# Optimization experiments

Hardware: AMD Instinct MI355X
Metric: run time of the kernel (lower is better)

Reference implementation:

```python
import jax, jax.numpy as jnp
import numpy as np

POOL_SIZE = 7
CROP = POOL_SIZE * 2  # if_max_pool=True -> crop to 14x14 then 2x2 max-pool


def setup_inputs() -> dict:
    key = jax.random.key(0)
    k1, k2, k3 = jax.random.split(key, 3)
    H, W, C = 50, 75, 512          # VGG conv5 features of an 800x1200 image (stride 16)
    N = 1000                       # post-NMS RPN proposals
    feature_map = jax.random.normal(k1, (1, H, W, C), dtype=jnp.float32)
    img_size = jnp.array([800, 1200], dtype=jnp.int32)
    # rois in pixel coords (x1, y1, x2, y2), guaranteed x1<=x2, y1<=y2, in-bounds
    xs = jax.random.uniform(k2, (N, 2), minval=0.0, maxval=1199.0)
    ys = jax.random.uniform(k3, (N, 2), minval=0.0, maxval=799.0)
    rois = jnp.stack([xs.min(1), ys.min(1), xs.max(1), ys.max(1)], axis=1).astype(jnp.float32)
    return {"feature_map": feature_map, "rois": rois, "img_size": img_size}


def _crop_and_resize(feature_map, boxes, crop_h, crop_w):
    """tf.image.crop_and_resize (bilinear) with all box_indices == 0.
    feature_map: (1,H,W,C); boxes: (N,4) normalized [y1,x1,y2,x2].
    Returns (N, crop_h, crop_w, C).
    """
    H, W = feature_map.shape[1], feature_map.shape[2]
    img = feature_map[0]  # (H,W,C)
    y1, x1, y2, x2 = boxes[:, 0], boxes[:, 1], boxes[:, 2], boxes[:, 3]
    fh, fw = jnp.float32(H - 1), jnp.float32(W - 1)
    iy = jnp.arange(crop_h, dtype=jnp.float32)
    ix = jnp.arange(crop_w, dtype=jnp.float32)
    # in-image sample coords (crop size > 1 branch of TF semantics)
    ys = y1[:, None] * fh + iy[None, :] * ((y2 - y1) * fh / (crop_h - 1))[:, None]  # (N,ch)
    xs = x1[:, None] * fw + ix[None, :] * ((x2 - x1) * fw / (crop_w - 1))[:, None]  # (N,cw)
    valid = ((ys >= 0) & (ys <= fh))[:, :, None] & ((xs >= 0) & (xs <= fw))[:, None, :]  # (N,ch,cw)
    y0 = jnp.floor(ys); x0 = jnp.floor(xs)
    wy = (ys - y0)[:, :, None, None]   # (N,ch,1,1)
    wx = (xs - x0)[:, None, :, None]   # (N,1,cw,1)
    y0i = jnp.clip(y0.astype(jnp.int32), 0, H - 1)
    x0i = jnp.clip(x0.astype(jnp.int32), 0, W - 1)
    y1i = jnp.clip(y0i + 1, 0, H - 1)
    x1i = jnp.clip(x0i + 1, 0, W - 1)
    # per-ROI bilinear gather: (N,ch,cw,C)
    tl = img[y0i[:, :, None], x0i[:, None, :]]
    tr = img[y0i[:, :, None], x1i[:, None, :]]
    bl = img[y1i[:, :, None], x0i[:, None, :]]
    br = img[y1i[:, :, None], x1i[:, None, :]]
    top = tl + wx * (tr - tl)
    bot = bl + wx * (br - bl)
    val = top + wy * (bot - top)
    return jnp.where(valid[..., None], val, 0.0)


def reference(feature_map, rois, img_size):
    img_h = img_size[0].astype(jnp.float32) - 1.0
    img_w = img_size[1].astype(jnp.float32) - 1.0
    boxes = jnp.stack([rois[:, 1] / img_h, rois[:, 0] / img_w,
                       rois[:, 3] / img_h, rois[:, 2] / img_w], axis=1)
    boxes = jax.lax.stop_gradient(boxes)
    crops = _crop_and_resize(feature_map, boxes, CROP, CROP)  # (N,14,14,C)
    N, _, _, C = crops.shape
    # MaxPool2D((2,2), padding='same'); 14 is even so 'same' == 'valid' reshape trick
    return crops.reshape(N, POOL_SIZE, 2, POOL_SIZE, 2, C).max(axis=(2, 4))
```

## Files before the change

### kernel.cpp

```cpp
#include <hip/hip_runtime.h>

#define FH 50
#define FW 75
#define FC 512
#define NPOOL 7
#define NXCD 8

typedef float f32x4 __attribute__((ext_vector_type(4)));

__device__ __forceinline__ float uniform_f(float x) {
    return __int_as_float(__builtin_amdgcn_readfirstlane(__float_as_int(x)));
}

__global__ __launch_bounds__(128) void roi_pool_kernel(
    const float* __restrict__ fmap,
    const float* __restrict__ rois,
    const int*   __restrict__ img_size,
    float* __restrict__ out,
    int N)
{
    const int nwg = gridDim.x;
    const int q = nwg / NXCD, r = nwg % NXCD;
    const int xcd = blockIdx.x % NXCD, local = blockIdx.x / NXCD;
    const int w = (xcd < r ? xcd * (q + 1) : r * (q + 1) + (xcd - r) * q) + local;

    const int n  = w / (NPOOL * NPOOL);
    const int p  = w % (NPOOL * NPOOL);
    const int py = p / NPOOL;
    const int px = p % NPOOL;
    if (n >= N) return;

    const float img_h = (float)(img_size[0] - 1);
    const float img_w = (float)(img_size[1] - 1);

    const float rx1 = rois[n * 4 + 0];
    const float ry1 = rois[n * 4 + 1];
    const float rx2 = rois[n * 4 + 2];
    const float ry2 = rois[n * 4 + 3];

    const float fh = (float)(FH - 1);
    const float fw = (float)(FW - 1);
    const float stepy = (ry2 - ry1) / img_h * fh * (1.0f / 13.0f);
    const float stepx = (rx2 - rx1) / img_w * fw * (1.0f / 13.0f);
    const float basey = ry1 / img_h * fh;
    const float basex = rx1 / img_w * fw;

    int   off00[4], off01[4], off10[4], off11[4];
    float w00_[4], w01_[4], w10_[4], w11_[4];
    #pragma unroll
    for (int kk = 0; kk < 4; ++kk) {
        const int iy = py * 2 + (kk >> 1);
        const int ix = px * 2 + (kk & 1);
        const float ys = basey + (float)iy * stepy;
        const float xs = basex + (float)ix * stepx;
        const float mv = ((ys >= 0.0f) & (ys <= fh) & (xs >= 0.0f) & (xs <= fw))
                         ? 1.0f : 0.0f;

        const float y0f = floorf(ys);
        const float x0f = floorf(xs);
        const float wy = ys - y0f;
        const float wx = xs - x0f;
        int y0i = (int)y0f; y0i = min(max(y0i, 0), FH - 1);
        int x0i = (int)x0f; x0i = min(max(x0i, 0), FW - 1);
        const int y1i = min(y0i + 1, FH - 1);
        const int x1i = min(x0i + 1, FW - 1);

        w00_[kk] = uniform_f((1.0f - wy) * (1.0f - wx) * mv);
        w01_[kk] = uniform_f((1.0f - wy) * wx * mv);
        w10_[kk] = uniform_f(wy * (1.0f - wx) * mv);
        w11_[kk] = uniform_f(wy * wx * mv);

        off00[kk] = __builtin_amdgcn_readfirstlane((y0i * FW + x0i) * FC);
        off01[kk] = __builtin_amdgcn_readfirstlane((y0i * FW + x1i) * FC);
        off10[kk] = __builtin_amdgcn_readfirstlane((y1i * FW + x0i) * FC);
        off11[kk] = __builtin_amdgcn_readfirstlane((y1i * FW + x1i) * FC);
    }

    const int c4 = threadIdx.x * 4;
    const float* fm = fmap + c4;

    f32x4 tl0, tr0, bl0, br0, tl1, tr1, bl1, br1;
    f32x4 tl2, tr2, bl2, br2, tl3, tr3, bl3, br3;
    tl0 = *(const f32x4*)(fm + off00[0]);
    tr0 = *(const f32x4*)(fm + off01[0]);
    bl0 = *(const f32x4*)(fm + off10[0]);
    br0 = *(const f32x4*)(fm + off11[0]);
    tl1 = *(const f32x4*)(fm + off00[1]);
    tr1 = *(const f32x4*)(fm + off01[1]);
    bl1 = *(const f32x4*)(fm + off10[1]);
    br1 = *(const f32x4*)(fm + off11[1]);
    tl2 = *(const f32x4*)(fm + off00[2]);
    tr2 = *(const f32x4*)(fm + off01[2]);
    bl2 = *(const f32x4*)(fm + off10[2]);
    br2 = *(const f32x4*)(fm + off11[2]);
    tl3 = *(const f32x4*)(fm + off00[3]);
    tr3 = *(const f32x4*)(fm + off01[3]);
    bl3 = *(const f32x4*)(fm + off10[3]);
    br3 = *(const f32x4*)(fm + off11[3]);

    asm volatile("" : "+v"(tl0), "+v"(tr0), "+v"(bl0), "+v"(br0),
                      "+v"(tl1), "+v"(tr1), "+v"(bl1), "+v"(br1),
                      "+v"(tl2), "+v"(tr2), "+v"(bl2), "+v"(br2),
                      "+v"(tl3), "+v"(tr3), "+v"(bl3), "+v"(br3));

    const f32x4 v0 = w00_[0] * tl0 + w01_[0] * tr0 + w10_[0] * bl0 + w11_[0] * br0;
    const f32x4 v1 = w00_[1] * tl1 + w01_[1] * tr1 + w10_[1] * bl1 + w11_[1] * br1;
    const f32x4 v2 = w00_[2] * tl2 + w01_[2] * tr2 + w10_[2] * bl2 + w11_[2] * br2;
    const f32x4 v3 = w00_[3] * tl3 + w01_[3] * tr3 + w10_[3] * bl3 + w11_[3] * br3;

    f32x4 m;
    m.x = fmaxf(fmaxf(fmaxf(v0.x, v1.x), v2.x), v3.x);
    m.y = fmaxf(fmaxf(fmaxf(v0.y, v1.y), v2.y), v3.y);
    m.z = fmaxf(fmaxf(fmaxf(v0.z, v1.z), v2.z), v3.z);
    m.w = fmaxf(fmaxf(fmaxf(v0.w, v1.w), v2.w), v3.w);

    f32x4* dst = (f32x4*)(out + (((long)n * NPOOL + py) * NPOOL + px) * FC + c4);
    __builtin_nontemporal_store(m, dst);
}

extern "C" void kernel_launch(void* const* d_in, const int* in_sizes, int n_in,
                              void* d_out, int out_size, void* d_ws, size_t ws_size,
                              hipStream_t stream) {
    const float* fmap     = (const float*)d_in[0];
    const float* rois     = (const float*)d_in[1];
    const int*   img_size = (const int*)d_in[2];
    float* out = (float*)d_out;

    const int N = in_sizes[1] / 4;
    const int blocks = N * NPOOL * NPOOL;
    roi_pool_kernel<<<blocks, 128, 0, stream>>>(fmap, rois, img_size, out, N);
}
```

Measured before the change: 159.4 us.

## Precompute separable per-ROI row/column sample tables in a setup kernel

```diff
diff --git a/kernel.cpp b/kernel.cpp
--- a/kernel.cpp
+++ b/kernel.cpp
@@ -5,17 +5,70 @@
 #define FC 512
 #define NPOOL 7
 #define NXCD 8
+#define NSAMP 14
 
 typedef float f32x4 __attribute__((ext_vector_type(4)));
+typedef int   i32x4 __attribute__((ext_vector_type(4)));
 
-__device__ __forceinline__ float uniform_f(float x) {
-    return __int_as_float(__builtin_amdgcn_readfirstlane(__float_as_int(x)));
+__global__ __launch_bounds__(256) void roi_setup_kernel(
+    const float* __restrict__ rois,
+    const int*   __restrict__ img_size,
+    i32x4* __restrict__ tab,
+    int N)
+{
+    const int idx = blockIdx.x * 256 + threadIdx.x;
+    const int total = N * NSAMP;
+    if (idx >= 2 * total) return;
+
+    const bool is_col = idx >= total;
+    const int  e = is_col ? idx - total : idx;
+    const int  n = e / NSAMP;
+    const int  j = e % NSAMP;
+
+    if (!is_col) {
+        const float img_h = (float)(img_size[0] - 1);
+        const float ry1 = rois[n * 4 + 1];
+        const float ry2 = rois[n * 4 + 3];
+        const float fh = (float)(FH - 1);
+        const float stepy = (ry2 - ry1) / img_h * fh * (1.0f / 13.0f);
+        const float basey = ry1 / img_h * fh;
+        const float ys = basey + (float)j * stepy;
+        const float my = ((ys >= 0.0f) & (ys <= fh)) ? 1.0f : 0.0f;
+        const float y0f = floorf(ys);
+        const float wy = ys - y0f;
+        int y0 = min(max((int)y0f, 0), FH - 1);
+        int y1 = min(y0 + 1, FH - 1);
+        i32x4 v;
+        v.x = y0 * (FW * FC);
+        v.y = y1 * (FW * FC);
+        v.z = __float_as_int((1.0f - wy) * my);
+        v.w = __float_as_int(wy * my);
+        tab[e] = v;
+    } else {
+        const float img_w = (float)(img_size[1] - 1);
+        const float rx1 = rois[n * 4 + 0];
+        const float rx2 = rois[n * 4 + 2];
+        const float fw = (float)(FW - 1);
+        const float stepx = (rx2 - rx1) / img_w * fw * (1.0f / 13.0f);
+        const float basex = rx1 / img_w * fw;
+        const float xs = basex + (float)j * stepx;
+        const float mx = ((xs >= 0.0f) & (xs <= fw)) ? 1.0f : 0.0f;
+        const float x0f = floorf(xs);
+        const float wx = xs - x0f;
+        int x0 = min(max((int)x0f, 0), FW - 1);
+        int x1 = min(x0 + 1, FW - 1);
+        i32x4 v;
+        v.x = x0 * FC;
+        v.y = x1 * FC;
+        v.z = __float_as_int((1.0f - wx) * mx);
+        v.w = __float_as_int(wx * mx);
+        tab[total + e] = v;
+    }
 }
 
 __global__ __launch_bounds__(128) void roi_pool_kernel(
     const float* __restrict__ fmap,
-    const float* __restrict__ rois,
-    const int*   __restrict__ img_size,
+    const i32x4* __restrict__ tab,
     float* __restrict__ out,
     int N)
 {
@@ -30,89 +83,48 @@
     const int px = p % NPOOL;
     if (n >= N) return;
 
-    const float img_h = (float)(img_size[0] - 1);
-    const float img_w = (float)(img_size[1] - 1);
+    const int ri = __builtin_amdgcn_readfirstlane(n * NSAMP + 2 * py);
+    const int ci = __builtin_amdgcn_readfirstlane(N * NSAMP + n * NSAMP + 2 * px);
+    const i32x4 R0 = tab[ri];
+    const i32x4 R1 = tab[ri + 1];
+    const i32x4 C0 = tab[ci];
+    const i32x4 C1 = tab[ci + 1];
 
-    const float rx1 = rois[n * 4 + 0];
-    const float ry1 = rois[n * 4 + 1];
-    const float rx2 = rois[n * 4 + 2];
-    const float ry2 = rois[n * 4 + 3];
-
-    const float fh = (float)(FH - 1);
-    const float fw = (float)(FW - 1);
-    const float stepy = (ry2 - ry1) / img_h * fh * (1.0f / 13.0f);
-    const float stepx = (rx2 - rx1) / img_w * fw * (1.0f / 13.0f);
-    const float basey = ry1 / img_h * fh;
-    const float basex = rx1 / img_w * fw;
-
-    int   off00[4], off01[4], off10[4], off11[4];
-    float w00_[4], w01_[4], w10_[4], w11_[4];
-    #pragma unroll
-    for (int kk = 0; kk < 4; ++kk) {
-        const int iy = py * 2 + (kk >> 1);
-        const int ix = px * 2 + (kk & 1);
-        const float ys = basey + (float)iy * stepy;
-        const float xs = basex + (float)ix * stepx;
-        const float mv = ((ys >= 0.0f) & (ys <= fh) & (xs >= 0.0f) & (xs <= fw))
-                         ? 1.0f : 0.0f;
-
-        const float y0f = floorf(ys);
-        const float x0f = floorf(xs);
-        const float wy = ys - y0f;
-        const float wx = xs - x0f;
-        int y0i = (int)y0f; y0i = min(max(y0i, 0), FH - 1);
-        int x0i = (int)x0f; x0i = min(max(x0i, 0), FW - 1);
-        const int y1i = min(y0i + 1, FH - 1);
-        const int x1i = min(x0i + 1, FW - 1);
-
-        w00_[kk] = uniform_f((1.0f - wy) * (1.0f - wx) * mv);
-        w01_[kk] = uniform_f((1.0f - wy) * wx * mv);
-        w10_[kk] = uniform_f(wy * (1.0f - wx) * mv);
-        w11_[kk] = uniform_f(wy * wx * mv);
-
-        off00[kk] = __builtin_amdgcn_readfirstlane((y0i * FW + x0i) * FC);
-        off01[kk] = __builtin_amdgcn_readfirstlane((y0i * FW + x1i) * FC);
-        off10[kk] = __builtin_amdgcn_readfirstlane((y1i * FW + x0i) * FC);
-        off11[kk] = __builtin_amdgcn_readfirstlane((y1i * FW + x1i) * FC);
-    }
+    const float r0a = __int_as_float(R0.z), r0b = __int_as_float(R0.w);
+    const float r1a = __int_as_float(R1.z), r1b = __int_as_float(R1.w);
+    const float c0a = __int_as_float(C0.z), c0b = __int_as_float(C0.w);
+    const float c1a = __int_as_float(C1.z), c1b = __int_as_float(C1.w);
 
     const int c4 = threadIdx.x * 4;
     const float* fm = fmap + c4;
 
-    f32x4 tl0, tr0, bl0, br0, tl1, tr1, bl1, br1;
-    f32x4 tl2, tr2, bl2, br2, tl3, tr3, bl3, br3;
-    tl0 = *(const f32x4*)(fm + off00[0]);
-    tr0 = *(const f32x4*)(fm + off01[0]);
-    bl0 = *(const f32x4*)(fm + off10[0]);
-    br0 = *(const f32x4*)(fm + off11[0]);
-    tl1 = *(const f32x4*)(fm + off00[1]);
-    tr1 = *(const f32x4*)(fm + off01[1]);
-    bl1 = *(const f32x4*)(fm + off10[1]);
-    br1 = *(const f32x4*)(fm + off11[1]);
-    tl2 = *(const f32x4*)(fm + off00[2]);
-    tr2 = *(const f32x4*)(fm + off01[2]);
-    bl2 = *(const f32x4*)(fm + off10[2]);
-    br2 = *(const f32x4*)(fm + off11[2]);
-    tl3 = *(const f32x4*)(fm + off00[3]);
-    tr3 = *(const f32x4*)(fm + off01[3]);
-    bl3 = *(const f32x4*)(fm + off10[3]);
-    br3 = *(const f32x4*)(fm + off11[3]);
+    const f32x4 s00a = *(const f32x4*)(fm + R0.x + C0.x);
+    const f32x4 s00b = *(const f32x4*)(fm + R0.x + C0.y);
+    const f32x4 s00c = *(const f32x4*)(fm + R0.y + C0.x);
+    const f32x4 s00d = *(const f32x4*)(fm + R0.y + C0.y);
+    const f32x4 s01a = *(const f32x4*)(fm + R0.x + C1.x);
+    const f32x4 s01b = *(const f32x4*)(fm + R0.x + C1.y);
+    const f32x4 s01c = *(const f32x4*)(fm + R0.y + C1.x);
+    const f32x4 s01d = *(const f32x4*)(fm + R0.y + C1.y);
+    const f32x4 s10a = *(const f32x4*)(fm + R1.x + C0.x);
+    const f32x4 s10b = *(const f32x4*)(fm + R1.x + C0.y);
+    const f32x4 s10c = *(const f32x4*)(fm + R1.y + C0.x);
+    const f32x4 s10d = *(const f32x4*)(fm + R1.y + C0.y);
+    const f32x4 s11a = *(const f32x4*)(fm + R1.x + C1.x);
+    const f32x4 s11b = *(const f32x4*)(fm + R1.x + C1.y);
+    const f32x4 s11c = *(const f32x4*)(fm + R1.y + C1.x);
+    const f32x4 s11d = *(const f32x4*)(fm + R1.y + C1.y);
 
-    asm volatile("" : "+v"(tl0), "+v"(tr0), "+v"(bl0), "+v"(br0),
-                      "+v"(tl1), "+v"(tr1), "+v"(bl1), "+v"(br1),
-                      "+v"(tl2), "+v"(tr2), "+v"(bl2), "+v"(br2),
-                      "+v"(tl3), "+v"(tr3), "+v"(bl3), "+v"(br3));
-
-    const f32x4 v0 = w00_[0] * tl0 + w01_[0] * tr0 + w10_[0] * bl0 + w11_[0] * br0;
-    const f32x4 v1 = w00_[1] * tl1 + w01_[1] * tr1 + w10_[1] * bl1 + w11_[1] * br1;
-    const f32x4 v2 = w00_[2] * tl2 + w01_[2] * tr2 + w10_[2] * bl2 + w11_[2] * br2;
-    const f32x4 v3 = w00_[3] * tl3 + w01_[3] * tr3 + w10_[3] * bl3 + w11_[3] * br3;
+    const f32x4 v00 = (r0a*c0a)*s00a + (r0a*c0b)*s00b + (r0b*c0a)*s00c + (r0b*c0b)*s00d;
+    const f32x4 v01 = (r0a*c1a)*s01a + (r0a*c1b)*s01b + (r0b*c1a)*s01c + (r0b*c1b)*s01d;
+    const f32x4 v10 = (r1a*c0a)*s10a + (r1a*c0b)*s10b + (r1b*c0a)*s10c + (r1b*c0b)*s10d;
+    const f32x4 v11 = (r1a*c1a)*s11a + (r1a*c1b)*s11b + (r1b*c1a)*s11c + (r1b*c1b)*s11d;
 
     f32x4 m;
-    m.x = fmaxf(fmaxf(fmaxf(v0.x, v1.x), v2.x), v3.x);
-    m.y = fmaxf(fmaxf(fmaxf(v0.y, v1.y), v2.y), v3.y);
-    m.z = fmaxf(fmaxf(fmaxf(v0.z, v1.z), v2.z), v3.z);
-    m.w = fmaxf(fmaxf(fmaxf(v0.w, v1.w), v2.w), v3.w);
+    m.x = fmaxf(fmaxf(fmaxf(v00.x, v01.x), v10.x), v11.x);
+    m.y = fmaxf(fmaxf(fmaxf(v00.y, v01.y), v10.y), v11.y);
+    m.z = fmaxf(fmaxf(fmaxf(v00.z, v01.z), v10.z), v11.z);
+    m.w = fmaxf(fmaxf(fmaxf(v00.w, v01.w), v10.w), v11.w);
 
     f32x4* dst = (f32x4*)(out + (((long)n * NPOOL + py) * NPOOL + px) * FC + c4);
     __builtin_nontemporal_store(m, dst);
@@ -127,6 +139,12 @@
     float* out = (float*)d_out;
 
     const int N = in_sizes[1] / 4;
+    i32x4* tab = (i32x4*)d_ws;
+
+    const int setup_threads = 2 * N * NSAMP;
+    roi_setup_kernel<<<(setup_threads + 255) / 256, 256, 0, stream>>>(
+        rois, img_size, tab, N);
+
     const int blocks = N * NPOOL * NPOOL;
-    roi_pool_kernel<<<blocks, 128, 0, stream>>>(fmap, rois, img_size, out, N);
+    roi_pool_kernel<<<blocks, 128, 0, stream>>>(fmap, tab, out, N);
 }
```

New measurement: 162.6 us. About the same (+2.0%).
